# Performance work log

Measured on AMD Instinct MI355X. Metric: run time of the kernel, lower is better.

Reference implementation:

```python
import jax, jax.numpy as jnp
import numpy as np

N, E, G = 50000, 600000, 512
F_IN, H, OUT = 128, 128, 256


def setup_inputs() -> dict:
    key = jax.random.key(0)
    ks = jax.random.split(key, 16)
    x = jax.random.normal(ks[0], (N, F_IN), dtype=jnp.float32)
    edge_index = jax.random.randint(ks[1], (2, E), 0, N, dtype=jnp.int64)
    batch = jnp.sort(jax.random.randint(ks[2], (N,), 0, G, dtype=jnp.int64))
    def lin(k, out_d, in_d):
        s = 1.0 / np.sqrt(in_d)
        return jax.random.uniform(k, (out_d, in_d), jnp.float32, -s, s)
    W1l, W1r = lin(ks[3], H, F_IN), lin(ks[4], H, F_IN)
    b1 = jnp.zeros((H,), jnp.float32)
    W2l, W2r = lin(ks[5], H, H), lin(ks[6], H, H)
    b2 = jnp.zeros((H,), jnp.float32)
    W3l, W3r = lin(ks[7], H, H), lin(ks[8], H, H)
    b3 = jnp.zeros((H,), jnp.float32)
    Wlin = lin(ks[9], OUT, 2 * H)
    blin = jnp.zeros((OUT,), jnp.float32)
    return dict(x=x, edge_index=edge_index, batch=batch,
                W1l=W1l, b1=b1, W1r=W1r, W2l=W2l, b2=b2, W2r=W2r,
                W3l=W3l, b3=b3, W3r=W3r, Wlin=Wlin, blin=blin)


def reference(x, edge_index, batch, W1l, b1, W1r, W2l, b2, W2r, W3l, b3, W3r, Wlin, blin):
    src, dst = edge_index[0], edge_index[1]
    # in-degree of each target node (mean aggregation denominator)
    deg = jax.ops.segment_sum(jnp.ones((E,), x.dtype), dst, num_segments=N)
    deg = jnp.maximum(deg, 1.0)[:, None]

    def sage(h, Wl, bl, Wr):
        # mean-aggregate neighbor features then linear; plus root transform
        agg = jax.ops.segment_sum(h[src], dst, num_segments=N) / deg
        return agg @ Wl.T + bl + h @ Wr.T

    h = jax.nn.relu(sage(x, W1l, b1, W1r))
    h = jax.nn.relu(sage(h, W2l, b2, W2r))
    h = sage(h, W3l, b3, W3r)

    # global max / mean pool per graph
    x_max = jax.ops.segment_max(h, batch, num_segments=G)
    x_max = jnp.where(jnp.isfinite(x_max), x_max, 0.0)
    cnt = jnp.maximum(jax.ops.segment_sum(jnp.ones((N,), h.dtype), batch, num_segments=G), 1.0)
    x_mean = jax.ops.segment_sum(h, batch, num_segments=G) / cnt[:, None]

    pooled = jnp.concatenate([x_max, x_mean], axis=1)  # [G, 2H]
    # dropout is identity in eval mode
    return pooled @ Wlin.T + blin
```

## Files before the change

### kernel.cpp

```cpp
#include <hip/hip_runtime.h>
#include <hip/hip_bf16.h>
#include <hip/hip_fp16.h>


#define FH 128
#define OUTD 256
#define SCHUNK 2048

typedef unsigned int u32;
typedef unsigned short u16;
typedef __attribute__((ext_vector_type(8))) _Float16 f16frag;
typedef __attribute__((ext_vector_type(4))) float f4frag;

typedef __attribute__((address_space(3))) u32 lds_u32;
typedef __attribute__((address_space(1))) const u32 glb_u32;

__device__ inline void async_copy16(const void* g, void* l) {
    __builtin_amdgcn_global_load_lds((glb_u32*)g, (lds_u32*)l, 16, 0, 0);
}

__global__ void hist_kernel(const int* __restrict__ dst, int* __restrict__ cnt, int E) {
    int e = blockIdx.x * 256 + threadIdx.x;
    if (e < E) atomicAdd(&cnt[dst[e]], 1);
}

__global__ void scanA_kernel(const int* __restrict__ cnt, int* __restrict__ bsum, int n) {
    __shared__ int ws[4];
    int b = blockIdx.x, t = threadIdx.x;
    int base = b * SCHUNK + t * 8;
    int s = 0;
    #pragma unroll
    for (int k = 0; k < 8; ++k) {
        int i = base + k;
        s += (i < n) ? cnt[i] : 0;
    }
    #pragma unroll
    for (int off = 32; off >= 1; off >>= 1) s += __shfl_xor(s, off, 64);
    int w = t >> 6, lane = t & 63;
    if (lane == 0) ws[w] = s;
    __syncthreads();
    if (t == 0) bsum[b] = ws[0] + ws[1] + ws[2] + ws[3];
}

__global__ void scanB_kernel(const int* __restrict__ bsum, int* __restrict__ boff,
                             int* __restrict__ rp, int B, int n) {
    int t = threadIdx.x;
    int v = (t < B) ? bsum[t] : 0;
    int x = v;
    #pragma unroll
    for (int off = 1; off < 64; off <<= 1) {
        int y = __shfl_up(x, off, 64);
        if (t >= off) x += y;
    }
    if (t < B) boff[t] = x - v;
    if (t == 63) rp[n] = x;
}

__global__ void scanC_kernel(const int* __restrict__ cnt, const int* __restrict__ boff,
                             int* __restrict__ rp, float* __restrict__ dinv, int n) {
    __shared__ int ws[4];
    int b = blockIdx.x, t = threadIdx.x;
    int base = b * SCHUNK + t * 8;
    int v[8];
    int ts = 0;
    #pragma unroll
    for (int k = 0; k < 8; ++k) {
        int i = base + k;
        v[k] = (i < n) ? cnt[i] : 0;
        ts += v[k];
    }
    int w = t >> 6, lane = t & 63;
    int x = ts;
    #pragma unroll
    for (int off = 1; off < 64; off <<= 1) {
        int y = __shfl_up(x, off, 64);
        if (lane >= off) x += y;
    }
    if (lane == 63) ws[w] = x;
    __syncthreads();
    int woff = 0;
    #pragma unroll
    for (int q = 0; q < 4; ++q) woff += (q < w) ? ws[q] : 0;
    int run = boff[b] + woff + (x - ts);
    #pragma unroll
    for (int k = 0; k < 8; ++k) {
        int i = base + k;
        if (i < n) {
            rp[i] = run;
            dinv[i] = 1.0f / (float)max(v[k], 1);
        }
        run += v[k];
    }
}

__global__ void scatter_kernel(const int* __restrict__ src, const int* __restrict__ dst,
                               const int* __restrict__ rp, int* __restrict__ cursor,
                               int* __restrict__ esrc, int E) {
    int e = blockIdx.x * 256 + threadIdx.x;
    if (e < E) {
        int d = dst[e];
        int pos = rp[d] + atomicAdd(&cursor[d], 1);
        esrc[pos] = src[e];
    }
}

__global__ void graph_bounds_kernel(const int* __restrict__ batch, int* __restrict__ gstart,
                                    int n, int g) {
    int i = blockIdx.x * 256 + threadIdx.x;
    if (i >= n) return;
    int b = batch[i];
    int pb = (i == 0) ? -1 : batch[i - 1];
    for (int q = pb + 1; q <= b; ++q) gstart[q] = i;
    if (i == n - 1) {
        for (int q = b + 1; q <= g; ++q) gstart[q] = n;
    }
}

__global__ void prep_x(const float* __restrict__ x, u16* __restrict__ x16, int n4) {
    int id = blockIdx.x * 256 + threadIdx.x;
    if (id >= n4) return;
    float4 v = *(const float4*)(x + (size_t)id * 4);
    __half h0 = __float2half(v.x), h1 = __float2half(v.y);
    __half h2 = __float2half(v.z), h3 = __float2half(v.w);
    ushort4 s;
    s.x = *(u16*)&h0; s.y = *(u16*)&h1; s.z = *(u16*)&h2; s.w = *(u16*)&h3;
    *(ushort4*)(x16 + (size_t)id * 4) = s;
}

__global__ void prep_w(const float* __restrict__ W0, const float* __restrict__ W1,
                       const float* __restrict__ W2, const float* __restrict__ W3,
                       const float* __restrict__ W4, const float* __restrict__ W5,
                       uint4* __restrict__ Bf) {
    const float* Ws[6] = {W0, W1, W2, W3, W4, W5};
    int ks = blockIdx.x;
    int arr = blockIdx.y;
    int l = threadIdx.x;
    const float* W = Ws[arr];
    bool use_lo = (ks >= 4);
    int kb = (ks & 3) * 32 + (l >> 4) * 8;
    uint4* out = Bf + (size_t)arr * 4096;
    #pragma unroll
    for (int ot = 0; ot < 8; ++ot) {
        int o = ot * 16 + (l & 15);
        u32 h[8];
        #pragma unroll
        for (int i = 0; i < 8; ++i) {
            float v = W[o * 128 + kb + i];
            __half hi = __float2half(v);
            if (use_lo) {
                float rem = v - __half2float(hi);
                __half lo = __float2half(rem);
                h[i] = *(u16*)&lo;
            } else {
                h[i] = *(u16*)&hi;
            }
        }
        uint4 u;
        u.x = h[0] | (h[1] << 16);
        u.y = h[2] | (h[3] << 16);
        u.z = h[4] | (h[5] << 16);
        u.w = h[6] | (h[7] << 16);
        out[(ks * 8 + ot) * 64 + l] = u;
    }
}

__device__ inline void add8(float* a, uint4 u) {
    float2 f0 = __half22float2(*(__half2*)&u.x);
    float2 f1 = __half22float2(*(__half2*)&u.y);
    float2 f2 = __half22float2(*(__half2*)&u.z);
    float2 f3 = __half22float2(*(__half2*)&u.w);
    a[0] += f0.x; a[1] += f0.y; a[2] += f1.x; a[3] += f1.y;
    a[4] += f2.x; a[5] += f2.y; a[6] += f3.x; a[7] += f3.y;
}

__global__ void agg_kernel(const u16* __restrict__ h16,
                           const int* __restrict__ rp, const int* __restrict__ esrc,
                           const float* __restrict__ dinv,
                           u16* __restrict__ agg16, int n_nodes) {
    int node = blockIdx.x * 16 + (threadIdx.x >> 4);
    if (node >= n_nodes) return;
    int lane = threadIdx.x & 15;
    int f = lane * 8;
    int s0 = rp[node], s1 = rp[node + 1];
    float a0[8] = {0, 0, 0, 0, 0, 0, 0, 0};
    float a1[8] = {0, 0, 0, 0, 0, 0, 0, 0};
    float a2[8] = {0, 0, 0, 0, 0, 0, 0, 0};
    float a3[8] = {0, 0, 0, 0, 0, 0, 0, 0};
    int j = s0;
    for (; j + 8 <= s1; j += 8) {
        int i0 = esrc[j],     i1 = esrc[j + 1], i2 = esrc[j + 2], i3 = esrc[j + 3];
        int i4 = esrc[j + 4], i5 = esrc[j + 5], i6 = esrc[j + 6], i7 = esrc[j + 7];
        uint4 u0 = *(const uint4*)(h16 + (size_t)i0 * FH + f);
        uint4 u1 = *(const uint4*)(h16 + (size_t)i1 * FH + f);
        uint4 u2 = *(const uint4*)(h16 + (size_t)i2 * FH + f);
        uint4 u3 = *(const uint4*)(h16 + (size_t)i3 * FH + f);
        uint4 u4 = *(const uint4*)(h16 + (size_t)i4 * FH + f);
        uint4 u5 = *(const uint4*)(h16 + (size_t)i5 * FH + f);
        uint4 u6 = *(const uint4*)(h16 + (size_t)i6 * FH + f);
        uint4 u7 = *(const uint4*)(h16 + (size_t)i7 * FH + f);
        add8(a0, u0); add8(a1, u1); add8(a2, u2); add8(a3, u3);
        add8(a0, u4); add8(a1, u5); add8(a2, u6); add8(a3, u7);
    }
    if (j + 4 <= s1) {
        int i0 = esrc[j], i1 = esrc[j + 1], i2 = esrc[j + 2], i3 = esrc[j + 3];
        uint4 u0 = *(const uint4*)(h16 + (size_t)i0 * FH + f);
        uint4 u1 = *(const uint4*)(h16 + (size_t)i1 * FH + f);
        uint4 u2 = *(const uint4*)(h16 + (size_t)i2 * FH + f);
        uint4 u3 = *(const uint4*)(h16 + (size_t)i3 * FH + f);
        add8(a0, u0); add8(a1, u1); add8(a2, u2); add8(a3, u3);
        j += 4;
    }
    for (; j < s1; ++j) {
        uint4 u0 = *(const uint4*)(h16 + (size_t)esrc[j] * FH + f);
        add8(a0, u0);
    }
    float di = dinv[node];
    u32 oh[8];
    #pragma unroll
    for (int i = 0; i < 8; ++i) {
        __half hv = __float2half((a0[i] + a1[i] + a2[i] + a3[i]) * di);
        oh[i] = *(u16*)&hv;
    }
    uint4 w;
    w.x = oh[0] | (oh[1] << 16);
    w.y = oh[2] | (oh[3] << 16);
    w.z = oh[4] | (oh[5] << 16);
    w.w = oh[6] | (oh[7] << 16);
    *(uint4*)(agg16 + (size_t)node * FH + f) = w;
}

__global__ __launch_bounds__(256, 2)
void mfma_gemm(const u16* __restrict__ A1, const u16* __restrict__ A2,
               const uint4* __restrict__ Bf1, const uint4* __restrict__ Bf2,
               const float* __restrict__ bias, u16* __restrict__ out16,
               int do_relu) {
    __shared__ uint4 Bl[4096];
    int tid = threadIdx.x;
    int l = tid & 63;
    int wv = tid >> 6;
    int bn0 = blockIdx.x * 192 + wv * 48;
    int m = l & 15, q = l >> 4;

    f4frag acc[3][8];
    #pragma unroll
    for (int i = 0; i < 3; ++i)
        #pragma unroll
        for (int o = 0; o < 8; ++o)
            acc[i][o] = (f4frag){0.f, 0.f, 0.f, 0.f};

    #pragma unroll
    for (int p = 0; p < 2; ++p) {
        const u16* P = p ? A2 : A1;
        const uint4* Bf = p ? Bf2 : Bf1;

        f16frag Af[3][4];
        #pragma unroll
        for (int nt = 0; nt < 3; ++nt)
            #pragma unroll
            for (int s = 0; s < 4; ++s)
                Af[nt][s] = *(const f16frag*)(P + (size_t)(bn0 + nt * 16 + m) * FH + s * 32 + q * 8);

        __syncthreads();

        #pragma unroll
        for (int u = 0; u < 16; ++u)
            async_copy16(Bf + (size_t)u * 256 + wv * 64 + l,
                         &Bl[u * 256 + wv * 64]);
        __syncthreads();

        #pragma unroll
        for (int s = 0; s < 4; ++s) {
            {
                f16frag B[8];
                #pragma unroll
                for (int ot = 0; ot < 8; ++ot)
                    B[ot] = *(const f16frag*)&Bl[(size_t)(s * 8 + ot) * 64 + l];
                #pragma unroll
                for (int ot = 0; ot < 8; ++ot)
                    #pragma unroll
                    for (int nt = 0; nt < 3; ++nt)
                        acc[nt][ot] = __builtin_amdgcn_mfma_f32_16x16x32_f16(Af[nt][s], B[ot], acc[nt][ot], 0, 0, 0);
            }
            {
                f16frag B[8];
                #pragma unroll
                for (int ot = 0; ot < 8; ++ot)
                    B[ot] = *(const f16frag*)&Bl[(size_t)((s + 4) * 8 + ot) * 64 + l];
                #pragma unroll
                for (int ot = 0; ot < 8; ++ot)
                    #pragma unroll
                    for (int nt = 0; nt < 3; ++nt)
                        acc[nt][ot] = __builtin_amdgcn_mfma_f32_16x16x32_f16(Af[nt][s], B[ot], acc[nt][ot], 0, 0, 0);
            }
        }
    }

    #pragma unroll
    for (int nt = 0; nt < 3; ++nt)
        #pragma unroll
        for (int r = 0; r < 4; ++r) {
            int node = bn0 + nt * 16 + q * 4 + r;
            #pragma unroll
            for (int ot = 0; ot < 8; ++ot) {
                float v = acc[nt][ot][r] + bias[ot * 16 + m];
                if (do_relu) v = fmaxf(v, 0.f);
                __half hv = __float2half(v);
                out16[(size_t)node * FH + ot * 16 + m] = *(u16*)&hv;
            }
        }
}

__global__ __launch_bounds__(256, 2)
void pool_final(const u16* __restrict__ h16, const int* __restrict__ gstart,
                const float* __restrict__ Wlin, const float* __restrict__ blin,
                float* __restrict__ out) {
    __shared__ float smax[16][FH];
    __shared__ float ssum[16][FH];
    __shared__ float pr[2 * FH];
    int g = blockIdx.x;
    int tid = threadIdx.x;
    int way = tid >> 4;
    int lane = tid & 15;
    int f = lane * 8;
    int s = gstart[g], e = gstart[g + 1];

    float mx[8], sm[8];
    #pragma unroll
    for (int i = 0; i < 8; ++i) { mx[i] = -INFINITY; sm[i] = 0.f; }
    for (int n = s + way; n < e; n += 16) {
        uint4 u = *(const uint4*)(h16 + (size_t)n * FH + f);
        float2 f0 = __half22float2(*(__half2*)&u.x);
        float2 f1 = __half22float2(*(__half2*)&u.y);
        float2 f2 = __half22float2(*(__half2*)&u.z);
        float2 f3 = __half22float2(*(__half2*)&u.w);
        float v[8] = {f0.x, f0.y, f1.x, f1.y, f2.x, f2.y, f3.x, f3.y};
        #pragma unroll
        for (int i = 0; i < 8; ++i) {
            mx[i] = fmaxf(mx[i], v[i]);
            sm[i] += v[i];
        }
    }
    #pragma unroll
    for (int i = 0; i < 8; ++i) {
        smax[way][f + i] = mx[i];
        ssum[way][f + i] = sm[i];
    }
    __syncthreads();
    int c = e - s;
    if (tid < FH) {
        float m2 = -INFINITY, s2 = 0.f;
        #pragma unroll
        for (int w2 = 0; w2 < 16; ++w2) {
            m2 = fmaxf(m2, smax[w2][tid]);
            s2 += ssum[w2][tid];
        }
        pr[tid] = (c > 0) ? m2 : 0.f;
        pr[FH + tid] = s2 / (float)max(c, 1);
    }
    __syncthreads();
    int o = tid;
    const float4* wr = (const float4*)(Wlin + (size_t)o * (2 * FH));
    float acc = 0.f;
    #pragma unroll
    for (int j = 0; j < (2 * FH) / 4; ++j) {
        float4 wv = wr[j];
        acc += wv.x * pr[j * 4 + 0] + wv.y * pr[j * 4 + 1] +
               wv.z * pr[j * 4 + 2] + wv.w * pr[j * 4 + 3];
    }
    out[(size_t)g * OUTD + o] = acc + blin[o];
}

extern "C" void kernel_launch(void* const* d_in, const int* in_sizes, int n_in,
                              void* d_out, int out_size, void* d_ws, size_t ws_size,
                              hipStream_t stream) {
    const float* x     = (const float*)d_in[0];
    const int*   ei    = (const int*)d_in[1];
    const int*   batch = (const int*)d_in[2];
    const float* W1l = (const float*)d_in[3];
    const float* b1  = (const float*)d_in[4];
    const float* W1r = (const float*)d_in[5];
    const float* W2l = (const float*)d_in[6];
    const float* b2  = (const float*)d_in[7];
    const float* W2r = (const float*)d_in[8];
    const float* W3l = (const float*)d_in[9];
    const float* b3  = (const float*)d_in[10];
    const float* W3r = (const float*)d_in[11];
    const float* Wlin = (const float*)d_in[12];
    const float* blin = (const float*)d_in[13];
    float* out = (float*)d_out;

    const int E = in_sizes[1] / 2;
    const int N = in_sizes[2];
    const int G = out_size / OUTD;
    const int* src = ei;
    const int* dst = ei + E;
    const int NB = (N + SCHUNK - 1) / SCHUNK;
    const int GB = (N + 191) / 192;
    const int NP = GB * 192;

    char* w = (char*)d_ws;
    auto alloc = [&](size_t bytes) {
        void* p = (void*)w;
        w += (bytes + 255) & ~(size_t)255;
        return p;
    };
    int*   cnt    = (int*)alloc((size_t)2 * N * sizeof(int));
    int*   cursor = cnt + N;
    int*   rp     = (int*)alloc((size_t)(N + 1) * sizeof(int));
    int*   esrc   = (int*)alloc((size_t)E * sizeof(int));
    int*   gstart = (int*)alloc((size_t)(G + 1) * sizeof(int));
    float* dinv   = (float*)alloc((size_t)N * sizeof(float));
    int*   bsum   = (int*)alloc(64 * sizeof(int));
    int*   boff   = (int*)alloc(64 * sizeof(int));
    u16*   x16    = (u16*)alloc((size_t)NP * FH * sizeof(u16));
    u16*   agg16  = (u16*)alloc((size_t)NP * FH * sizeof(u16));
    u16*   hA16   = (u16*)alloc((size_t)NP * FH * sizeof(u16));
    u16*   hB16   = (u16*)alloc((size_t)NP * FH * sizeof(u16));
    uint4* BF     = (uint4*)alloc((size_t)6 * 4096 * sizeof(uint4));
    (void)ws_size;

    prep_x<<<(N * 32 + 255) / 256, 256, 0, stream>>>(x, x16, N * 32);
    prep_w<<<dim3(8, 6), 64, 0, stream>>>(W1l, W1r, W2l, W2r, W3l, W3r, BF);

    hipMemsetAsync(cnt, 0, (size_t)2 * N * sizeof(int), stream);
    hist_kernel<<<(E + 255) / 256, 256, 0, stream>>>(dst, cnt, E);
    scanA_kernel<<<NB, 256, 0, stream>>>(cnt, bsum, N);
    scanB_kernel<<<1, 64, 0, stream>>>(bsum, boff, rp, NB, N);
    scanC_kernel<<<NB, 256, 0, stream>>>(cnt, boff, rp, dinv, N);
    scatter_kernel<<<(E + 255) / 256, 256, 0, stream>>>(src, dst, rp, cursor, esrc, E);
    graph_bounds_kernel<<<(N + 255) / 256, 256, 0, stream>>>(batch, gstart, N, G);

    const int agg_grid = (N + 15) / 16;

    agg_kernel<<<agg_grid, 256, 0, stream>>>(x16, rp, esrc, dinv, agg16, N);
    mfma_gemm<<<GB, 256, 0, stream>>>(agg16, x16, BF + 0 * 4096, BF + 1 * 4096, b1, hA16, 1);
    agg_kernel<<<agg_grid, 256, 0, stream>>>(hA16, rp, esrc, dinv, agg16, N);
    mfma_gemm<<<GB, 256, 0, stream>>>(agg16, hA16, BF + 2 * 4096, BF + 3 * 4096, b2, hB16, 1);
    agg_kernel<<<agg_grid, 256, 0, stream>>>(hB16, rp, esrc, dinv, agg16, N);
    mfma_gemm<<<GB, 256, 0, stream>>>(agg16, hB16, BF + 4 * 4096, BF + 5 * 4096, b3, hA16, 0);

    pool_final<<<G, 256, 0, stream>>>(hA16, gstart, Wlin, blin, out);
}
```

Measured before the change: 334.6 us.

## Fuse CSR build and input prep into one cooperative grid-synced kernel

Merges memset, x/W fp16 conversion, degree histogram, the three-stage scan, the edge scatter and the graph-bounds computation into a single cooperative kernel with grid.sync barriers. The block-offset scan now lets each scan block reduce bsum itself rather than running a separate single-block kernel. The goal is to remove roughly ten kernel launches and their gaps. In exchange it adds grid-wide barriers and limits the grid to 512 persistent blocks. It also leaves behind an unused, broken csr_coop variant containing dead code.

```diff
diff --git a/kernel.cpp b/kernel.cpp
--- a/kernel.cpp
+++ b/kernel.cpp
@@ -1,11 +1,15 @@
 #include <hip/hip_runtime.h>
 #include <hip/hip_bf16.h>
 #include <hip/hip_fp16.h>
+#include <hip/hip_cooperative_groups.h>
 
 
 #define FH 128
 #define OUTD 256
 #define SCHUNK 2048
+#define CSRG 512
+
+namespace cg = cooperative_groups;
 
 typedef unsigned int u32;
 typedef unsigned short u16;
@@ -19,148 +23,302 @@
     __builtin_amdgcn_global_load_lds((glb_u32*)g, (lds_u32*)l, 16, 0, 0);
 }
 
-__global__ void hist_kernel(const int* __restrict__ dst, int* __restrict__ cnt, int E) {
-    int e = blockIdx.x * 256 + threadIdx.x;
-    if (e < E) atomicAdd(&cnt[dst[e]], 1);
-}
-
-__global__ void scanA_kernel(const int* __restrict__ cnt, int* __restrict__ bsum, int n) {
+__global__ __launch_bounds__(256, 2)
+void csr_coop(const float* __restrict__ x, u16* __restrict__ x16, int n4,
+              const float* __restrict__ W0, const float* __restrict__ W1,
+              const float* __restrict__ W2, const float* __restrict__ W3,
+              const float* __restrict__ W4, const float* __restrict__ W5,
+              uint4* __restrict__ Bf,
+              const int* __restrict__ src, const int* __restrict__ dst,
+              int* __restrict__ cnt, int* __restrict__ cursor, int E, int n, int NB,
+              int* __restrict__ rp, float* __restrict__ dinv, int* __restrict__ bsum,
+              const int* __restrict__ batch, int* __restrict__ gstart, int g) {
+    cg::grid_group grid = cg::this_grid();
     __shared__ int ws[4];
-    int b = blockIdx.x, t = threadIdx.x;
-    int base = b * SCHUNK + t * 8;
-    int s = 0;
-    #pragma unroll
-    for (int k = 0; k < 8; ++k) {
-        int i = base + k;
-        s += (i < n) ? cnt[i] : 0;
-    }
-    #pragma unroll
-    for (int off = 32; off >= 1; off >>= 1) s += __shfl_xor(s, off, 64);
-    int w = t >> 6, lane = t & 63;
-    if (lane == 0) ws[w] = s;
-    __syncthreads();
-    if (t == 0) bsum[b] = ws[0] + ws[1] + ws[2] + ws[3];
-}
-
-__global__ void scanB_kernel(const int* __restrict__ bsum, int* __restrict__ boff,
-                             int* __restrict__ rp, int B, int n) {
+    __shared__ int base_s;
     int t = threadIdx.x;
-    int v = (t < B) ? bsum[t] : 0;
-    int x = v;
-    #pragma unroll
-    for (int off = 1; off < 64; off <<= 1) {
-        int y = __shfl_up(x, off, 64);
-        if (t >= off) x += y;
-    }
-    if (t < B) boff[t] = x - v;
-    if (t == 63) rp[n] = x;
-}
-
-__global__ void scanC_kernel(const int* __restrict__ cnt, const int* __restrict__ boff,
-                             int* __restrict__ rp, float* __restrict__ dinv, int n) {
+    int gtid = blockIdx.x * 256 + t;
+    int stride = gridDim.x * 256;
+
+    for (int i = gtid; i < 2 * n; i += stride) cnt[i] = 0;
+    grid.sync();
+
+    for (int i = gtid; i < n4; i += stride) {
+        float4 v = *(const float4*)(x + (size_t)i * 4);
+        __half h0 = __float2half(v.x), h1 = __float2half(v.y);
+        __half h2 = __float2half(v.z), h3 = __float2half(v.w);
+        ushort4 s;
+        s.x = *(u16*)&h0; s.y = *(u16*)&h1; s.z = *(u16*)&h2; s.w = *(u16*)&h3;
+        *(ushort4*)(x16 + (size_t)i * 4) = s;
+    }
+    {
+        int wid = gtid >> 6;
+        if (wid < 48) {
+            int ks = wid & 7;
+            int arr = wid >> 3;
+            int l = gtid & 63;
+            const float* Ws[6] = {W0, W1, W2, W3, W4, W5};
+            const float* W = Ws[arr];
+            bool use_lo = (ks >= 4);
+            int kb = (ks & 3) * 32 + (l >> 4) * 8;
+            uint4* out = Bf + (size_t)arr * 4096;
+            #pragma unroll
+            for (int ot = 0; ot < 8; ++ot) {
+                int o = ot * 16 + (l & 15);
+                u32 h[8];
+                #pragma unroll
+                for (int i = 0; i < 8; ++i) {
+                    float v = W[o * 128 + kb + i];
+                    __half hi = __float2half(v);
+                    if (use_lo) {
+                        float rem = v - __half2float(hi);
+                        __half lo = __float2half(rem);
+                        h[i] = *(u16*)&lo;
+                    } else {
+                        h[i] = *(u16*)&hi;
+                    }
+                }
+                uint4 u;
+                u.x = h[0] | (h[1] << 16);
+                u.y = h[2] | (h[3] << 16);
+                u.z = h[4] | (h[5] << 16);
+                u.w = h[6] | (h[7] << 16);
+                out[(ks * 8 + ot) * 64 + l] = u;
+            }
+        }
+    }
+    for (int e = gtid; e < E; e += stride) atomicAdd(&cnt[dst[e]], 1);
+    grid.sync();
+
+    if ((int)blockIdx.x < NB) {
+        int b = blockIdx.x;
+        int base = b * SCHUNK + t * 8;
+        int s = 0;
+        #pragma unroll
+        for (int k = 0; k < 8; ++k) {
+            int i = base + k;
+            s += (i < n) ? cnt[i] : 0;
+        }
+        #pragma unroll
+        for (int off = 32; off >= 1; off >>= 1) s += __shfl_xor(s, off, 64);
+        int w = t >> 6, lane = t & 63;
+        if (lane == 0) ws[w] = s;
+        __syncthreads();
+        if (t == 0) bsum[b] = ws[0] + ws[1] + ws[2] + ws[3];
+    }
+    grid.sync();
+
+    if ((int)blockIdx.x < NB) {
+        int b = blockIdx.x;
+        if (t < 64) {
+            int v = (t < NB) ? bsum[t] : 0;
+            int pre = (t < b) ? v : 0;
+            #pragma unroll
+            for (int off = 32; off >= 1; off >>= 1) pre += __shfl_xor(pre, off, 64);
+            if (t == 0) base_s = pre;
+            if (b == 0) {
+                int tot = v;
+                #pragma unroll
+                for (int off = 32; off >= 1; off >>= 1) tot += __shfl_xor(tot, off, 64);
+                if (t == 0) rp[n] = tot;
+            }
+        }
+        __syncthreads();
+        int boff = base_s;
+        int base = b * SCHUNK + t * 8;
+        int v[8];
+        int ts = 0;
+        #pragma unroll
+        for (int k = 0; k < 8; ++k) {
+            int i = base + k;
+            v[k] = (i < n) ? cnt[i] : 0;
+            ts += v[k];
+        }
+        int w = t >> 6, lane = t & 63;
+        int x2 = ts;
+        #pragma unroll
+        for (int off = 1; off < 64; off <<= 1) {
+            int y = __shfl_up(x2, off, 64);
+            if (lane >= off) x2 += y;
+        }
+        if (lane == 63) ws[w] = x2;
+        __syncthreads();
+        int woff = 0;
+        #pragma unroll
+        for (int q = 0; q < 4; ++q) woff += (q < w) ? ws[q] : 0;
+        int run = boff + woff + (x2 - ts);
+        #pragma unroll
+        for (int k = 0; k < 8; ++k) {
+            int i = base + k;
+            if (i < n) {
+                rp[i] = run;
+                dinv[i] = 1.0f / (float)max(v[k], 1);
+            }
+            run += v[k];
+        }
+    }
+    grid.sync();
+
+    for (int e = gtid; e < E; e += stride) {
+        int d = dst[e];
+        int pos = rp[d] + atomicAdd(&cursor[d], 1);
+        esrc_write:
+        ((int*)cursor)[0] = ((int*)cursor)[0];
+        (void)pos;
+        break;
+    }
+    grid.sync();
+}
+
+__global__ __launch_bounds__(256, 2)
+void csr_coop2(const float* __restrict__ x, u16* __restrict__ x16, int n4,
+               const float* __restrict__ W0, const float* __restrict__ W1,
+               const float* __restrict__ W2, const float* __restrict__ W3,
+               const float* __restrict__ W4, const float* __restrict__ W5,
+               uint4* __restrict__ Bf,
+               const int* __restrict__ src, const int* __restrict__ dst,
+               int* __restrict__ cnt, int* __restrict__ cursor,
+               int* __restrict__ esrc, int E, int n, int NB,
+               int* __restrict__ rp, float* __restrict__ dinv, int* __restrict__ bsum,
+               const int* __restrict__ batch, int* __restrict__ gstart, int g) {
+    cg::grid_group grid = cg::this_grid();
     __shared__ int ws[4];
-    int b = blockIdx.x, t = threadIdx.x;
-    int base = b * SCHUNK + t * 8;
-    int v[8];
-    int ts = 0;
-    #pragma unroll
-    for (int k = 0; k < 8; ++k) {
-        int i = base + k;
-        v[k] = (i < n) ? cnt[i] : 0;
-        ts += v[k];
-    }
-    int w = t >> 6, lane = t & 63;
-    int x = ts;
-    #pragma unroll
-    for (int off = 1; off < 64; off <<= 1) {
-        int y = __shfl_up(x, off, 64);
-        if (lane >= off) x += y;
-    }
-    if (lane == 63) ws[w] = x;
-    __syncthreads();
-    int woff = 0;
-    #pragma unroll
-    for (int q = 0; q < 4; ++q) woff += (q < w) ? ws[q] : 0;
-    int run = boff[b] + woff + (x - ts);
-    #pragma unroll
-    for (int k = 0; k < 8; ++k) {
-        int i = base + k;
-        if (i < n) {
-            rp[i] = run;
-            dinv[i] = 1.0f / (float)max(v[k], 1);
-        }
-        run += v[k];
-    }
-}
-
-__global__ void scatter_kernel(const int* __restrict__ src, const int* __restrict__ dst,
-                               const int* __restrict__ rp, int* __restrict__ cursor,
-                               int* __restrict__ esrc, int E) {
-    int e = blockIdx.x * 256 + threadIdx.x;
-    if (e < E) {
+    __shared__ int base_s;
+    int t = threadIdx.x;
+    int gtid = blockIdx.x * 256 + t;
+    int stride = gridDim.x * 256;
+
+    for (int i = gtid; i < 2 * n; i += stride) cnt[i] = 0;
+    grid.sync();
+
+    for (int i = gtid; i < n4; i += stride) {
+        float4 v = *(const float4*)(x + (size_t)i * 4);
+        __half h0 = __float2half(v.x), h1 = __float2half(v.y);
+        __half h2 = __float2half(v.z), h3 = __float2half(v.w);
+        ushort4 s;
+        s.x = *(u16*)&h0; s.y = *(u16*)&h1; s.z = *(u16*)&h2; s.w = *(u16*)&h3;
+        *(ushort4*)(x16 + (size_t)i * 4) = s;
+    }
+    {
+        int wid = gtid >> 6;
+        if (wid < 48) {
+            int ks = wid & 7;
+            int arr = wid >> 3;
+            int l = gtid & 63;
+            const float* Ws[6] = {W0, W1, W2, W3, W4, W5};
+            const float* W = Ws[arr];
+            bool use_lo = (ks >= 4);
+            int kb = (ks & 3) * 32 + (l >> 4) * 8;
+            uint4* out = Bf + (size_t)arr * 4096;
+            #pragma unroll
+            for (int ot = 0; ot < 8; ++ot) {
+                int o = ot * 16 + (l & 15);
+                u32 h[8];
+                #pragma unroll
+                for (int i = 0; i < 8; ++i) {
+                    float v = W[o * 128 + kb + i];
+                    __half hi = __float2half(v);
+                    if (use_lo) {
+                        float rem = v - __half2float(hi);
+                        __half lo = __float2half(rem);
+                        h[i] = *(u16*)&lo;
+                    } else {
+                        h[i] = *(u16*)&hi;
+                    }
+                }
+                uint4 u;
+                u.x = h[0] | (h[1] << 16);
+                u.y = h[2] | (h[3] << 16);
+                u.z = h[4] | (h[5] << 16);
+                u.w = h[6] | (h[7] << 16);
+                out[(ks * 8 + ot) * 64 + l] = u;
+            }
+        }
+    }
+    for (int e = gtid; e < E; e += stride) atomicAdd(&cnt[dst[e]], 1);
+    grid.sync();
+
+    if ((int)blockIdx.x < NB) {
+        int b = blockIdx.x;
+        int base = b * SCHUNK + t * 8;
+        int s = 0;
+        #pragma unroll
+        for (int k = 0; k < 8; ++k) {
+            int i = base + k;
+            s += (i < n) ? cnt[i] : 0;
+        }
+        #pragma unroll
+        for (int off = 32; off >= 1; off >>= 1) s += __shfl_xor(s, off, 64);
+        int w = t >> 6, lane = t & 63;
+        if (lane == 0) ws[w] = s;
+        __syncthreads();
+        if (t == 0) bsum[b] = ws[0] + ws[1] + ws[2] + ws[3];
+    }
+    grid.sync();
+
+    if ((int)blockIdx.x < NB) {
+        int b = blockIdx.x;
+        if (t < 64) {
+            int v = (t < NB) ? bsum[t] : 0;
+            int pre = (t < b) ? v : 0;
+            #pragma unroll
+            for (int off = 32; off >= 1; off >>= 1) pre += __shfl_xor(pre, off, 64);
+            if (t == 0) base_s = pre;
+            if (b == 0) {
+                int tot = v;
+                #pragma unroll
+                for (int off = 32; off >= 1; off >>= 1) tot += __shfl_xor(tot, off, 64);
+                if (t == 0) rp[n] = tot;
+            }
+        }
+        __syncthreads();
+        int boff = base_s;
+        int base = b * SCHUNK + t * 8;
+        int v[8];
+        int ts = 0;
+        #pragma unroll
+        for (int k = 0; k < 8; ++k) {
+            int i = base + k;
+            v[k] = (i < n) ? cnt[i] : 0;
+            ts += v[k];
+        }
+        int w = t >> 6, lane = t & 63;
+        int x2 = ts;
+        #pragma unroll
+        for (int off = 1; off < 64; off <<= 1) {
+            int y = __shfl_up(x2, off, 64);
+            if (lane >= off) x2 += y;
+        }
+        if (lane == 63) ws[w] = x2;
+        __syncthreads();
+        int woff = 0;
+        #pragma unroll
+        for (int q = 0; q < 4; ++q) woff += (q < w) ? ws[q] : 0;
+        int run = boff + woff + (x2 - ts);
+        #pragma unroll
+        for (int k = 0; k < 8; ++k) {
+            int i = base + k;
+            if (i < n) {
+                rp[i] = run;
+                dinv[i] = 1.0f / (float)max(v[k], 1);
+            }
+            run += v[k];
+        }
+    }
+    grid.sync();
+
+    for (int e = gtid; e < E; e += stride) {
         int d = dst[e];
         int pos = rp[d] + atomicAdd(&cursor[d], 1);
         esrc[pos] = src[e];
     }
-}
-
-__global__ void graph_bounds_kernel(const int* __restrict__ batch, int* __restrict__ gstart,
-                                    int n, int g) {
-    int i = blockIdx.x * 256 + threadIdx.x;
-    if (i >= n) return;
-    int b = batch[i];
-    int pb = (i == 0) ? -1 : batch[i - 1];
-    for (int q = pb + 1; q <= b; ++q) gstart[q] = i;
-    if (i == n - 1) {
-        for (int q = b + 1; q <= g; ++q) gstart[q] = n;
-    }
-}
-
-__global__ void prep_x(const float* __restrict__ x, u16* __restrict__ x16, int n4) {
-    int id = blockIdx.x * 256 + threadIdx.x;
-    if (id >= n4) return;
-    float4 v = *(const float4*)(x + (size_t)id * 4);
-    __half h0 = __float2half(v.x), h1 = __float2half(v.y);
-    __half h2 = __float2half(v.z), h3 = __float2half(v.w);
-    ushort4 s;
-    s.x = *(u16*)&h0; s.y = *(u16*)&h1; s.z = *(u16*)&h2; s.w = *(u16*)&h3;
-    *(ushort4*)(x16 + (size_t)id * 4) = s;
-}
-
-__global__ void prep_w(const float* __restrict__ W0, const float* __restrict__ W1,
-                       const float* __restrict__ W2, const float* __restrict__ W3,
-                       const float* __restrict__ W4, const float* __restrict__ W5,
-                       uint4* __restrict__ Bf) {
-    const float* Ws[6] = {W0, W1, W2, W3, W4, W5};
-    int ks = blockIdx.x;
-    int arr = blockIdx.y;
-    int l = threadIdx.x;
-    const float* W = Ws[arr];
-    bool use_lo = (ks >= 4);
-    int kb = (ks & 3) * 32 + (l >> 4) * 8;
-    uint4* out = Bf + (size_t)arr * 4096;
-    #pragma unroll
-    for (int ot = 0; ot < 8; ++ot) {
-        int o = ot * 16 + (l & 15);
-        u32 h[8];
-        #pragma unroll
-        for (int i = 0; i < 8; ++i) {
-            float v = W[o * 128 + kb + i];
-            __half hi = __float2half(v);
-            if (use_lo) {
-                float rem = v - __half2float(hi);
-                __half lo = __float2half(rem);
-                h[i] = *(u16*)&lo;
-            } else {
-                h[i] = *(u16*)&hi;
-            }
-        }
-        uint4 u;
-        u.x = h[0] | (h[1] << 16);
-        u.y = h[2] | (h[3] << 16);
-        u.z = h[4] | (h[5] << 16);
-        u.w = h[6] | (h[7] << 16);
-        out[(ks * 8 + ot) * 64 + l] = u;
+    for (int i = gtid; i < n; i += stride) {
+        int b = batch[i];
+        int pb = (i == 0) ? -1 : batch[i - 1];
+        for (int q = pb + 1; q <= b; ++q) gstart[q] = i;
+        if (i == n - 1) {
+            for (int q = b + 1; q <= g; ++q) gstart[q] = n;
+        }
     }
 }
 
@@ -411,7 +569,6 @@
     int*   gstart = (int*)alloc((size_t)(G + 1) * sizeof(int));
     float* dinv   = (float*)alloc((size_t)N * sizeof(float));
     int*   bsum   = (int*)alloc(64 * sizeof(int));
-    int*   boff   = (int*)alloc(64 * sizeof(int));
     u16*   x16    = (u16*)alloc((size_t)NP * FH * sizeof(u16));
     u16*   agg16  = (u16*)alloc((size_t)NP * FH * sizeof(u16));
     u16*   hA16   = (u16*)alloc((size_t)NP * FH * sizeof(u16));
@@ -419,16 +576,21 @@
     uint4* BF     = (uint4*)alloc((size_t)6 * 4096 * sizeof(uint4));
     (void)ws_size;
 
-    prep_x<<<(N * 32 + 255) / 256, 256, 0, stream>>>(x, x16, N * 32);
-    prep_w<<<dim3(8, 6), 64, 0, stream>>>(W1l, W1r, W2l, W2r, W3l, W3r, BF);
-
-    hipMemsetAsync(cnt, 0, (size_t)2 * N * sizeof(int), stream);
-    hist_kernel<<<(E + 255) / 256, 256, 0, stream>>>(dst, cnt, E);
-    scanA_kernel<<<NB, 256, 0, stream>>>(cnt, bsum, N);
-    scanB_kernel<<<1, 64, 0, stream>>>(bsum, boff, rp, NB, N);
-    scanC_kernel<<<NB, 256, 0, stream>>>(cnt, boff, rp, dinv, N);
-    scatter_kernel<<<(E + 255) / 256, 256, 0, stream>>>(src, dst, rp, cursor, esrc, E);
-    graph_bounds_kernel<<<(N + 255) / 256, 256, 0, stream>>>(batch, gstart, N, G);
+    int n4 = N * 32;
+    int Ev = E, Nv = N, NBv = NB, Gv = G;
+    const float* W0 = W1l; const float* W1_ = W1r; const float* W2_ = W2l;
+    const float* W3_ = W2r; const float* W4_ = W3l; const float* W5_ = W3r;
+    void* args[] = {
+        (void*)&x, (void*)&x16, (void*)&n4,
+        (void*)&W0, (void*)&W1_, (void*)&W2_, (void*)&W3_, (void*)&W4_, (void*)&W5_,
+        (void*)&BF,
+        (void*)&src, (void*)&dst,
+        (void*)&cnt, (void*)&cursor, (void*)&esrc,
+        (void*)&Ev, (void*)&Nv, (void*)&NBv,
+        (void*)&rp, (void*)&dinv, (void*)&bsum,
+        (void*)&batch, (void*)&gstart, (void*)&Gv
+    };
+    hipLaunchCooperativeKernel((void*)csr_coop2, dim3(CSRG), dim3(256), args, 0, stream);
 
     const int agg_grid = (N + 15) / 16;
 
```

Measured after the change: 543.7 us. +62.5%, slower.
